# Performance work log

Hardware: AMD Instinct MI355X
Metric: run time of the kernel (lower is better)

The kernel has to match this reference:

```python
import jax, jax.numpy as jnp
import numpy as np


def _reflect(x, size):
    # PyTorch grid_sample reflection padding, align_corners=False:
    # reflect about borders at -0.5 and size-0.5, then clip to [0, size-1].
    x = x + 0.5
    x = jnp.mod(x, 2.0 * size)
    x = jnp.where(x >= size, 2.0 * size - x, x)
    x = x - 0.5
    return jnp.clip(x, 0.0, size - 1.0)


def _grid_sample_one(img, grid):
    # img: (H, W, C); grid: (H, W, 2) with (x, y) in [-1, 1]
    H, W, _ = img.shape
    # unnormalize, align_corners=False
    ix = ((grid[..., 0] + 1.0) * W - 1.0) * 0.5
    iy = ((grid[..., 1] + 1.0) * H - 1.0) * 0.5
    ix = _reflect(ix, W)
    iy = _reflect(iy, H)
    x0 = jnp.floor(ix)
    y0 = jnp.floor(iy)
    wx = (ix - x0)[..., None]
    wy = (iy - y0)[..., None]
    x0i = jnp.clip(x0, 0, W - 1).astype(jnp.int32)
    x1i = jnp.clip(x0 + 1.0, 0, W - 1).astype(jnp.int32)
    y0i = jnp.clip(y0, 0, H - 1).astype(jnp.int32)
    y1i = jnp.clip(y0 + 1.0, 0, H - 1).astype(jnp.int32)
    Ia = img[y0i, x0i]  # (H, W, C)
    Ib = img[y0i, x1i]
    Ic = img[y1i, x0i]
    Id = img[y1i, x1i]
    return (Ia * (1 - wx) * (1 - wy) + Ib * wx * (1 - wy)
            + Ic * (1 - wx) * wy + Id * wx * wy)


def _displace(image, displacement_map, amplitude, angle):
    N, H, W, C = image.shape
    # base sampling grid, torch.linspace(-1, 1, size) endpoints included
    gy, gx = jnp.meshgrid(jnp.linspace(-1.0, 1.0, H, dtype=image.dtype),
                          jnp.linspace(-1.0, 1.0, W, dtype=image.dtype),
                          indexing='ij')
    base = jnp.stack([gx, gy], axis=-1)  # (H, W, 2) as (x, y)
    # bilinear resize (half-pixel centers == torch align_corners=False)
    dm = jax.image.resize(displacement_map,
                          (N, H, W, displacement_map.shape[-1]),
                          method='bilinear')
    if dm.shape[-1] == 3:
        dm = jnp.mean(dm, axis=-1)  # (N, H, W)
    else:
        dm = dm[..., 0]
    d = dm * amplitude[:, None, None]
    dx = jnp.cos(angle)[:, None, None] * d / (W - 1) * 2.0
    dy = jnp.sin(angle)[:, None, None] * d / (H - 1) * 2.0
    grid = base[None] + jnp.stack([dx, dy], axis=-1)  # (N, H, W, 2)
    return jax.vmap(_grid_sample_one)(image, grid)  # (N, H, W, C)


def setup_inputs() -> dict:
    key = jax.random.key(0)
    k1, k2, k3, k4 = jax.random.split(key, 4)
    N, H, W, C = 8, 1024, 1024, 3
    image = jax.random.normal(k1, (N, H, W, C), dtype=jnp.float32)
    displacement_map = jax.random.uniform(k2, (N, 512, 512, 3), dtype=jnp.float32)
    amplitude = jax.random.uniform(k3, (N,), dtype=jnp.float32) * 20.0  # pixels
    angle = jax.random.uniform(k4, (N,), dtype=jnp.float32) * 2.0 * np.pi
    return {"image": image, "displacement_map": displacement_map,
            "amplitude": amplitude, "angle": angle}


def reference(image, displacement_map, amplitude, angle):
    return _displace(image, displacement_map, amplitude, angle)
```

## Files before the change

### kernel.cpp

```cpp
#include <hip/hip_runtime.h>
#include <math.h>
#include <limits.h>

typedef float f4u __attribute__((ext_vector_type(4), aligned(4)));
typedef float f2u __attribute__((ext_vector_type(2), aligned(4)));

#define TILE_W 64
#define TILE_H 16
#define XB 88
#define YB 38
#define XBF (XB * 3)

__device__ __forceinline__ float reflect_pre(float xr, float size, float two, float inv_two) {
    xr = xr - floorf(xr * inv_two) * two;
    if (xr >= size) xr = two - xr;
    xr -= 0.5f;
    return fminf(fmaxf(xr, 0.0f), size - 1.0f);
}

__device__ __forceinline__ void px_taps(int w, int h, float dm,
    float cW, float cH, float kxc, float kyc, int W, int H,
    float twoW, float twoH, float invTwoW, float invTwoH,
    int& qx, int& jy0, int& jy1, float& wx, float& wy, bool& cl)
{
    float rx = (float)w * cW + dm * kxc;
    float ry = (float)h * cH + dm * kyc;
    float ix = reflect_pre(rx, (float)W, twoW, invTwoW);
    float iy = reflect_pre(ry, (float)H, twoH, invTwoH);
    float x0f = floorf(ix), y0f = floorf(iy);
    wx = ix - x0f;  wy = iy - y0f;
    int ix0 = (int)x0f;
    jy0 = (int)y0f;
    jy1 = min(jy0 + 1, H - 1);
    qx  = min(ix0, W - 2);
    cl  = (ix0 > qx);
}

__global__ __launch_bounds__(256, 4) void displace_tile_kernel(
    const float* __restrict__ img,
    const float* __restrict__ dmap,
    const float* __restrict__ amp,
    const float* __restrict__ ang,
    float* __restrict__ out,
    int N, int H, int W, int DH, int DW,
    int tiles_x, int tiles_per_img, unsigned nb)
{
    __shared__ __align__(16) float band[YB * XBF];

    unsigned id  = blockIdx.x;
    unsigned q   = nb >> 3, r = nb & 7u;
    unsigned xcd = id & 7u, off = id >> 3;
    unsigned orig = (xcd < r) ? (xcd * (q + 1u) + off)
                              : (r * (q + 1u) + (xcd - r) * q + off);

    int n    = (int)(orig / (unsigned)tiles_per_img);
    int rem  = (int)(orig % (unsigned)tiles_per_img);
    int ty_t = rem / tiles_x;
    int tx_t = rem % tiles_x;

    int lane = (int)(threadIdx.x & 63u);
    int warp = (int)(threadIdx.x >> 6u);

    int x0 = tx_t * TILE_W;
    int hT = ty_t * TILE_H;
    int w  = x0 + lane;
    int h0 = hT + warp * 4;

    int M  = h0 >> 1;
    int fx = (w >> 1) - 1 + (w & 1);
    float txd = (w & 1) ? 0.25f : 0.75f;
    int qd = min(max(fx, 0), DW - 2);
    bool hiA = (fx >= DW - 1);
    bool loB = (fx < 0);

    const float* dbase = dmap + (long long)n * DH * DW * 3;
    f4u dv[4]; f2u du[4];
    #pragma unroll
    for (int j = 0; j < 4; ++j) {
        int rj = min(max(M - 1 + j, 0), DH - 1);
        const float* pr = dbase + ((long long)rj * DW + qd) * 3;
        dv[j] = *(const f4u*)pr;
        du[j] = *(const f2u*)(pr + 4);
    }

    float a = amp[n];
    float sa, ca;
    sincosf(ang[n], &sa, &ca);
    float cW = (float)W / (float)(W - 1);
    float cH = (float)H / (float)(H - 1);
    float kxc = ca * a * cW;
    float kyc = sa * a * cH;
    float twoW = 2.0f * (float)W, twoH = 2.0f * (float)H;
    float invTwoW = 1.0f / twoW, invTwoH = 1.0f / twoH;
    const float s3 = 1.0f / 3.0f;

    float ixmin = (float)x0 * cW - 0.5f + fminf(0.0f, kxc);
    float ixmax = (float)(x0 + TILE_W - 1) * cW - 0.5f + fmaxf(0.0f, kxc);
    float iymin = (float)hT * cH - 0.5f + fminf(0.0f, kyc);
    float iymax = (float)(hT + TILE_H - 1) * cH - 0.5f + fmaxf(0.0f, kyc);

    int xlo = (int)floorf(ixmin);
    int xhi = (int)floorf(ixmax) + 1;
    if (ixmin < -0.5f)            xhi = max(xhi, (int)floorf(-ixmin - 1.0f) + 1);
    if (ixmax > (float)W - 0.5f)  xlo = min(xlo, (int)floorf(twoW - ixmax - 1.0f));
    xlo = max(0, xlo);  xhi = min(W - 1, xhi);

    int ylo = (int)floorf(iymin);
    int yhi = (int)floorf(iymax) + 1;
    if (iymin < -0.5f)            yhi = max(yhi, (int)floorf(-iymin - 1.0f) + 1);
    if (iymax > (float)H - 0.5f)  ylo = min(ylo, (int)floorf(twoH - iymax - 1.0f));
    ylo = max(0, ylo);  yhi = min(H - 1, yhi);

    int cols  = xhi - xlo + 1;
    int colsp = (cols + 3) & ~3;
    int rowsn = yhi - ylo + 1;
    bool ok = (colsp <= XB) && (rowsn <= YB) && (colsp <= W);

    const float* ibase = img + (long long)n * H * W * 3;

    float Rr[4];
    #pragma unroll
    for (int j = 0; j < 4; ++j) {
        float mlo = dv[j].x + dv[j].y + dv[j].z;
        float mhi = dv[j].w + du[j].x + du[j].y;
        float A = hiA ? mhi : mlo;
        float B = loB ? mlo : mhi;
        Rr[j] = A + txd * (B - A);
    }
    const int   jlo[4] = {0, 1, 1, 2};
    const float tyv[4] = {0.75f, 0.25f, 0.75f, 0.25f};

    long long obase = ((long long)(n * H + h0) * W + w) * 3;

    if (ok) {
        xlo = min(xlo, W - colsp);

        int chunks = (colsp * 3) >> 2;
        for (int row = warp; row < rowsn; row += 4) {
            const float* g = ibase + ((long long)(ylo + row) * W + xlo) * 3;
            float* l = band + row * XBF;
            for (int c = lane; c < chunks; c += 64) {
                f4u v = *(const f4u*)(g + 4 * c);
                float4 t; t.x = v.x; t.y = v.y; t.z = v.z; t.w = v.w;
                *(float4*)(l + 4 * c) = t;
            }
        }
        __syncthreads();

        int b0[4], b1[4]; float wxv[4], wyv[4]; bool CL[4];
        #pragma unroll
        for (int p = 0; p < 4; ++p) {
            float Ra = Rr[jlo[p]], Rb = Rr[jlo[p] + 1];
            float dm = (Ra + tyv[p] * (Rb - Ra)) * s3;
            int qx, jy0, jy1; float wx, wy; bool cl;
            px_taps(w, h0 + p, dm, cW, cH, kxc, kyc, W, H,
                    twoW, twoH, invTwoW, invTwoH, qx, jy0, jy1, wx, wy, cl);
            int ldx = min(max(qx - xlo, 0), colsp - 2);
            int ly0 = min(max(jy0 - ylo, 0), rowsn - 1);
            int ly1 = min(max(jy1 - ylo, 0), rowsn - 1);
            b0[p] = ly0 * XBF + ldx * 3;
            b1[p] = ly1 * XBF + ldx * 3;
            wxv[p] = wx; wyv[p] = wy; CL[p] = cl;
        }

        float t0[4][6], t1[4][6];
        #pragma unroll
        for (int p = 0; p < 4; ++p) {
            #pragma unroll
            for (int j = 0; j < 6; ++j) {
                t0[p][j] = band[b0[p] + j];
                t1[p][j] = band[b1[p] + j];
            }
        }

        #pragma unroll
        for (int p = 0; p < 4; ++p) {
            float wx = wxv[p], wy = wyv[p];
            float wa = (1.0f - wx) * (1.0f - wy);
            float wb = wx * (1.0f - wy);
            float wc = (1.0f - wx) * wy;
            float wd = wx * wy;
            bool cl = CL[p];
            float A0 = cl ? t0[p][3] : t0[p][0], A1 = cl ? t0[p][4] : t0[p][1], A2 = cl ? t0[p][5] : t0[p][2];
            float B0 = t0[p][3],                 B1 = t0[p][4],                 B2 = t0[p][5];
            float C0 = cl ? t1[p][3] : t1[p][0], C1 = cl ? t1[p][4] : t1[p][1], C2 = cl ? t1[p][5] : t1[p][2];
            float D0 = t1[p][3],                 D1 = t1[p][4],                 D2 = t1[p][5];
            float* o = out + obase + (long long)p * W * 3;
            o[0] = A0 * wa + B0 * wb + C0 * wc + D0 * wd;
            o[1] = A1 * wa + B1 * wb + C1 * wc + D1 * wd;
            o[2] = A2 * wa + B2 * wb + C2 * wc + D2 * wd;
        }
    } else {
        #pragma unroll
        for (int p = 0; p < 4; ++p) {
            float Ra = Rr[jlo[p]], Rb = Rr[jlo[p] + 1];
            float dm = (Ra + tyv[p] * (Rb - Ra)) * s3;
            int qx, jy0, jy1; float wx, wy; bool cl;
            px_taps(w, h0 + p, dm, cW, cH, kxc, kyc, W, H,
                    twoW, twoH, invTwoW, invTwoH, qx, jy0, jy1, wx, wy, cl);
            const float* PA = ibase + ((long long)jy0 * W + qx) * 3;
            const float* PB = ibase + ((long long)jy1 * W + qx) * 3;
            f4u va = *(const f4u*)PA;  f2u ua = *(const f2u*)(PA + 4);
            f4u vb = *(const f4u*)PB;  f2u ub = *(const f2u*)(PB + 4);
            float wa = (1.0f - wx) * (1.0f - wy);
            float wb = wx * (1.0f - wy);
            float wc = (1.0f - wx) * wy;
            float wd = wx * wy;
            float A0 = cl ? va.w : va.x, A1 = cl ? ua.x : va.y, A2 = cl ? ua.y : va.z;
            float B0 = va.w,             B1 = ua.x,             B2 = ua.y;
            float C0 = cl ? vb.w : vb.x, C1 = cl ? ub.x : vb.y, C2 = cl ? ub.y : vb.z;
            float D0 = vb.w,             D1 = ub.x,             D2 = ub.y;
            float* o = out + obase + (long long)p * W * 3;
            o[0] = A0 * wa + B0 * wb + C0 * wc + D0 * wd;
            o[1] = A1 * wa + B1 * wb + C1 * wc + D1 * wd;
            o[2] = A2 * wa + B2 * wb + C2 * wc + D2 * wd;
        }
    }
}

__device__ __forceinline__ float reflect_coord(float x, float size) {
    x += 0.5f;
    float two = 2.0f * size;
    x = x - floorf(x / two) * two;
    if (x >= size) x = two - x;
    x -= 0.5f;
    return fminf(fmaxf(x, 0.0f), size - 1.0f);
}

__global__ __launch_bounds__(256) void displace_kernel(
    const float* __restrict__ img, const float* __restrict__ dmap,
    const float* __restrict__ amp, const float* __restrict__ ang,
    float* __restrict__ out, int N, int H, int W, int DH, int DW)
{
    long long idx = (long long)blockIdx.x * blockDim.x + threadIdx.x;
    long long total = (long long)N * H * W;
    if (idx >= total) return;
    int w = (int)(idx % W);
    long long t = idx / W;
    int h = (int)(t % H);
    int n = (int)(t / H);

    float sx = (w + 0.5f) * ((float)DW / (float)W) - 0.5f;
    float sy = (h + 0.5f) * ((float)DH / (float)H) - 0.5f;
    float fx = floorf(sx), fy = floorf(sy);
    float tx = sx - fx, ty = sy - fy;
    int dx0 = max(0, min(DW - 1, (int)fx));
    int dx1 = max(0, min(DW - 1, (int)fx + 1));
    int dy0 = max(0, min(DH - 1, (int)fy));
    int dy1 = max(0, min(DH - 1, (int)fy + 1));

    const float* dbase = dmap + (long long)n * DH * DW * 3;
    const float* p00 = dbase + ((long long)dy0 * DW + dx0) * 3;
    const float* p01 = dbase + ((long long)dy0 * DW + dx1) * 3;
    const float* p10 = dbase + ((long long)dy1 * DW + dx0) * 3;
    const float* p11 = dbase + ((long long)dy1 * DW + dx1) * 3;
    float m00 = p00[0] + p00[1] + p00[2];
    float m01 = p01[0] + p01[1] + p01[2];
    float m10 = p10[0] + p10[1] + p10[2];
    float m11 = p11[0] + p11[1] + p11[2];
    float dmv = ((m00 * (1.0f - tx) + m01 * tx) * (1.0f - ty)
               + (m10 * (1.0f - tx) + m11 * tx) * ty) * (1.0f / 3.0f);

    float a = amp[n];
    float sa, ca;
    sincosf(ang[n], &sa, &ca);
    float d = dmv * a;
    float ddx = ca * d * (2.0f / (float)(W - 1));
    float ddy = sa * d * (2.0f / (float)(H - 1));
    float gx = -1.0f + 2.0f * (float)w / (float)(W - 1) + ddx;
    float gy = -1.0f + 2.0f * (float)h / (float)(H - 1) + ddy;
    float ix = ((gx + 1.0f) * (float)W - 1.0f) * 0.5f;
    float iy = ((gy + 1.0f) * (float)H - 1.0f) * 0.5f;
    ix = reflect_coord(ix, (float)W);
    iy = reflect_coord(iy, (float)H);

    float x0f = floorf(ix), y0f = floorf(iy);
    float wx = ix - x0f, wy = iy - y0f;
    int ix0 = min((int)x0f, W - 1);
    int ix1 = min((int)x0f + 1, W - 1);
    int iy0 = min((int)y0f, H - 1);
    int iy1 = min((int)y0f + 1, H - 1);

    const float* ibase = img + (long long)n * H * W * 3;
    const float* Ia = ibase + ((long long)iy0 * W + ix0) * 3;
    const float* Ib = ibase + ((long long)iy0 * W + ix1) * 3;
    const float* Ic = ibase + ((long long)iy1 * W + ix0) * 3;
    const float* Id = ibase + ((long long)iy1 * W + ix1) * 3;
    float wa = (1.0f - wx) * (1.0f - wy);
    float wb = wx * (1.0f - wy);
    float wc = (1.0f - wx) * wy;
    float wd = wx * wy;
    float* o = out + idx * 3;
    #pragma unroll
    for (int c = 0; c < 3; ++c)
        o[c] = Ia[c] * wa + Ib[c] * wb + Ic[c] * wc + Id[c] * wd;
}

extern "C" void kernel_launch(void* const* d_in, const int* in_sizes, int n_in,
                              void* d_out, int out_size, void* d_ws, size_t ws_size,
                              hipStream_t stream) {
    const float* img  = (const float*)d_in[0];
    const float* dmap = (const float*)d_in[1];
    const float* amp  = (const float*)d_in[2];
    const float* ang  = (const float*)d_in[3];
    float* out = (float*)d_out;

    int N = in_sizes[2];
    long long hw  = (long long)in_sizes[0] / ((long long)N * 3);
    int H = (int)llround(sqrt((double)hw));
    int W = H;
    long long dhw = (long long)in_sizes[1] / ((long long)N * 3);
    int DH = (int)llround(sqrt((double)dhw));
    int DW = DH;

    bool fast = (W % 64 == 0) && (H % 16 == 0) && (W == 2 * DW) && (H == 2 * DH) &&
                (DW >= 2) && ((long long)H * W <= (long long)INT_MAX);

    if (fast) {
        int tiles_x = W / 64;
        int tiles_y = H / 16;
        int tpi = tiles_x * tiles_y;
        unsigned nb = (unsigned)((long long)tpi * N);
        displace_tile_kernel<<<nb, 256, 0, stream>>>(
            img, dmap, amp, ang, out, N, H, W, DH, DW, tiles_x, tpi, nb);
    } else {
        long long total = (long long)N * H * W;
        int block = 256;
        long long grid = (total + block - 1) / block;
        displace_kernel<<<(dim3)(unsigned)grid, block, 0, stream>>>(
            img, dmap, amp, ang, out, N, H, W, DH, DW);
    }
}
```

Before: 225.7 us.

## Use 512-thread blocks with fixed-size shared band and two rows per wave

Each block now runs 512 threads, so a wave handles two output rows instead of four, and fewer displacement-map rows are loaded per thread. The shared-memory band load becomes a fixed-size, unrolled 92x38 window with no inner loop or variable column count. Output stores are partially vectorised into 8-byte writes. The aim is more parallelism per tile and cheaper, more regular band staging, at the cost of loading some unneeded band pixels and higher per-block thread counts.

New measurement: 240.2 us. +6.4%, slower.

```diff
diff --git a/kernel.cpp b/kernel.cpp
--- a/kernel.cpp
+++ b/kernel.cpp
@@ -7,9 +7,9 @@
 
 #define TILE_W 64
 #define TILE_H 16
-#define XB 88
 #define YB 38
-#define XBF (XB * 3)
+#define XBT 92
+#define XBF (XBT * 3)
 
 __device__ __forceinline__ float reflect_pre(float xr, float size, float two, float inv_two) {
     xr = xr - floorf(xr * inv_two) * two;
@@ -36,7 +36,7 @@
     cl  = (ix0 > qx);
 }
 
-__global__ __launch_bounds__(256, 4) void displace_tile_kernel(
+__global__ __launch_bounds__(512, 8) void displace_tile_kernel(
     const float* __restrict__ img,
     const float* __restrict__ dmap,
     const float* __restrict__ amp,
@@ -64,7 +64,7 @@
     int x0 = tx_t * TILE_W;
     int hT = ty_t * TILE_H;
     int w  = x0 + lane;
-    int h0 = hT + warp * 4;
+    int h0 = hT + warp * 2;
 
     int M  = h0 >> 1;
     int fx = (w >> 1) - 1 + (w & 1);
@@ -74,9 +74,9 @@
     bool loB = (fx < 0);
 
     const float* dbase = dmap + (long long)n * DH * DW * 3;
-    f4u dv[4]; f2u du[4];
+    f4u dv[3]; f2u du[3];
     #pragma unroll
-    for (int j = 0; j < 4; ++j) {
+    for (int j = 0; j < 3; ++j) {
         int rj = min(max(M - 1 + j, 0), DH - 1);
         const float* pr = dbase + ((long long)rj * DW + qd) * 3;
         dv[j] = *(const f4u*)pr;
@@ -112,60 +112,63 @@
     ylo = max(0, ylo);  yhi = min(H - 1, yhi);
 
     int cols  = xhi - xlo + 1;
-    int colsp = (cols + 3) & ~3;
     int rowsn = yhi - ylo + 1;
-    bool ok = (colsp <= XB) && (rowsn <= YB) && (colsp <= W);
+    bool ok = (cols <= XBT - 4) && (rowsn <= YB);
 
     const float* ibase = img + (long long)n * H * W * 3;
 
-    float Rr[4];
+    float Rr[3];
     #pragma unroll
-    for (int j = 0; j < 4; ++j) {
+    for (int j = 0; j < 3; ++j) {
         float mlo = dv[j].x + dv[j].y + dv[j].z;
         float mhi = dv[j].w + du[j].x + du[j].y;
         float A = hiA ? mhi : mlo;
         float B = loB ? mlo : mhi;
         Rr[j] = A + txd * (B - A);
     }
-    const int   jlo[4] = {0, 1, 1, 2};
-    const float tyv[4] = {0.75f, 0.25f, 0.75f, 0.25f};
-
-    long long obase = ((long long)(n * H + h0) * W + w) * 3;
+    const float tyv[2] = {0.75f, 0.25f};
 
     if (ok) {
-        xlo = min(xlo, W - colsp);
-
-        int chunks = (colsp * 3) >> 2;
-        for (int row = warp; row < rowsn; row += 4) {
-            const float* g = ibase + ((long long)(ylo + row) * W + xlo) * 3;
-            float* l = band + row * XBF;
-            for (int c = lane; c < chunks; c += 64) {
-                f4u v = *(const f4u*)(g + 4 * c);
-                float4 t; t.x = v.x; t.y = v.y; t.z = v.z; t.w = v.w;
-                *(float4*)(l + 4 * c) = t;
+        int xlo_f = xlo & ~3;
+        xlo_f = min(xlo_f, W - XBT);
+        xlo_f = max(xlo_f, 0);
+        int ylo_f = min(ylo, H - YB);
+        ylo_f = max(ylo_f, 0);
+
+        const float* gb = ibase + ((long long)ylo_f * W + xlo_f) * 3;
+        #pragma unroll
+        for (int rr = 0; rr < 5; ++rr) {
+            int row = warp + rr * 8;
+            if (row < YB) {
+                const float* g = gb + (long long)row * W * 3;
+                float* l = band + row * XBF;
+                *(float4*)(l + 4 * lane) = *(const float4*)(g + 4 * lane);
+                if (lane < (XBF / 4 - 64)) {
+                    *(float4*)(l + 256 + 4 * lane) = *(const float4*)(g + 256 + 4 * lane);
+                }
             }
         }
         __syncthreads();
 
-        int b0[4], b1[4]; float wxv[4], wyv[4]; bool CL[4];
-        #pragma unroll
-        for (int p = 0; p < 4; ++p) {
-            float Ra = Rr[jlo[p]], Rb = Rr[jlo[p] + 1];
+        int b0[2], b1[2]; float wxv[2], wyv[2]; bool CL[2];
+        #pragma unroll
+        for (int p = 0; p < 2; ++p) {
+            float Ra = Rr[p], Rb = Rr[p + 1];
             float dm = (Ra + tyv[p] * (Rb - Ra)) * s3;
             int qx, jy0, jy1; float wx, wy; bool cl;
             px_taps(w, h0 + p, dm, cW, cH, kxc, kyc, W, H,
                     twoW, twoH, invTwoW, invTwoH, qx, jy0, jy1, wx, wy, cl);
-            int ldx = min(max(qx - xlo, 0), colsp - 2);
-            int ly0 = min(max(jy0 - ylo, 0), rowsn - 1);
-            int ly1 = min(max(jy1 - ylo, 0), rowsn - 1);
+            int ldx = min(max(qx - xlo_f, 0), XBT - 2);
+            int ly0 = min(max(jy0 - ylo_f, 0), YB - 1);
+            int ly1 = min(max(jy1 - ylo_f, 0), YB - 1);
             b0[p] = ly0 * XBF + ldx * 3;
             b1[p] = ly1 * XBF + ldx * 3;
             wxv[p] = wx; wyv[p] = wy; CL[p] = cl;
         }
 
-        float t0[4][6], t1[4][6];
-        #pragma unroll
-        for (int p = 0; p < 4; ++p) {
+        float t0[2][6], t1[2][6];
+        #pragma unroll
+        for (int p = 0; p < 2; ++p) {
             #pragma unroll
             for (int j = 0; j < 6; ++j) {
                 t0[p][j] = band[b0[p] + j];
@@ -174,7 +177,7 @@
         }
 
         #pragma unroll
-        for (int p = 0; p < 4; ++p) {
+        for (int p = 0; p < 2; ++p) {
             float wx = wxv[p], wy = wyv[p];
             float wa = (1.0f - wx) * (1.0f - wy);
             float wb = wx * (1.0f - wy);
@@ -185,15 +188,16 @@
             float B0 = t0[p][3],                 B1 = t0[p][4],                 B2 = t0[p][5];
             float C0 = cl ? t1[p][3] : t1[p][0], C1 = cl ? t1[p][4] : t1[p][1], C2 = cl ? t1[p][5] : t1[p][2];
             float D0 = t1[p][3],                 D1 = t1[p][4],                 D2 = t1[p][5];
-            float* o = out + obase + (long long)p * W * 3;
-            o[0] = A0 * wa + B0 * wb + C0 * wc + D0 * wd;
-            o[1] = A1 * wa + B1 * wb + C1 * wc + D1 * wd;
+            float* o = out + (((long long)(n * H + h0 + p)) * W + w) * 3;
+            f2u s2; s2.x = A0 * wa + B0 * wb + C0 * wc + D0 * wd;
+            s2.y = A1 * wa + B1 * wb + C1 * wc + D1 * wd;
+            *(f2u*)o = s2;
             o[2] = A2 * wa + B2 * wb + C2 * wc + D2 * wd;
         }
     } else {
         #pragma unroll
-        for (int p = 0; p < 4; ++p) {
-            float Ra = Rr[jlo[p]], Rb = Rr[jlo[p] + 1];
+        for (int p = 0; p < 2; ++p) {
+            float Ra = Rr[p], Rb = Rr[p + 1];
             float dm = (Ra + tyv[p] * (Rb - Ra)) * s3;
             int qx, jy0, jy1; float wx, wy; bool cl;
             px_taps(w, h0 + p, dm, cW, cH, kxc, kyc, W, H,
@@ -210,9 +214,10 @@
             float B0 = va.w,             B1 = ua.x,             B2 = ua.y;
             float C0 = cl ? vb.w : vb.x, C1 = cl ? ub.x : vb.y, C2 = cl ? ub.y : vb.z;
             float D0 = vb.w,             D1 = ub.x,             D2 = ub.y;
-            float* o = out + obase + (long long)p * W * 3;
-            o[0] = A0 * wa + B0 * wb + C0 * wc + D0 * wd;
-            o[1] = A1 * wa + B1 * wb + C1 * wc + D1 * wd;
+            float* o = out + (((long long)(n * H + h0 + p)) * W + w) * 3;
+            f2u s2; s2.x = A0 * wa + B0 * wb + C0 * wc + D0 * wd;
+            s2.y = A1 * wa + B1 * wb + C1 * wc + D1 * wd;
+            *(f2u*)o = s2;
             o[2] = A2 * wa + B2 * wb + C2 * wc + D2 * wd;
         }
     }
@@ -314,14 +319,15 @@
     int DW = DH;
 
     bool fast = (W % 64 == 0) && (H % 16 == 0) && (W == 2 * DW) && (H == 2 * DH) &&
-                (DW >= 2) && ((long long)H * W <= (long long)INT_MAX);
+                (DW >= 2) && (W >= 128) && (H >= 64) &&
+                ((long long)H * W <= (long long)INT_MAX);
 
     if (fast) {
-        int tiles_x = W / 64;
-        int tiles_y = H / 16;
+        int tiles_x = W / TILE_W;
+        int tiles_y = H / TILE_H;
         int tpi = tiles_x * tiles_y;
         unsigned nb = (unsigned)((long long)tpi * N);
-        displace_tile_kernel<<<nb, 256, 0, stream>>>(
+        displace_tile_kernel<<<nb, 512, 0, stream>>>(
             img, dmap, amp, ang, out, N, H, W, DH, DW, tiles_x, tpi, nb);
     } else {
         long long total = (long long)N * H * W;
```
